# Optimization experiments

Measured on AMD Instinct MI355X. Metric: run time of the kernel, lower is better.

The kernel has to match this reference:

```python
import jax, jax.numpy as jnp
import numpy as np

EPS = 1e-12  # F.normalize eps

def _l2norm(v, axis):
    n = jnp.sqrt(jnp.sum(v * v, axis=axis, keepdims=True))
    return v / jnp.maximum(n, EPS)

def setup_inputs() -> dict:
    key = jax.random.key(0)
    k1, k2, k3, k4 = jax.random.split(key, 4)
    B, C, H, W, K = 8, 1024, 64, 64, 64
    x = jax.random.normal(k1, (B, C, H, W), dtype=jnp.float32)
    centroids = jax.random.normal(k2, (K, C), dtype=jnp.float32)
    # 1x1 conv initialized to identity in the module; use random perturbed weights for a non-trivial test
    fc_weight = jax.random.normal(k3, (C, C), dtype=jnp.float32) * 0.02 + jnp.eye(C, dtype=jnp.float32)
    fc_bias = jax.random.normal(k4, (C,), dtype=jnp.float32) * 0.01
    return {"x": x, "centroids": centroids, "fc_weight": fc_weight, "fc_bias": fc_bias}

def reference(x, centroids, fc_weight, fc_bias):
    B, C, H, W = x.shape
    K = centroids.shape[0]
    # Eq.1: nearest-centroid assignment via cosine similarity
    x_n = _l2norm(x, axis=1)            # [B,C,H,W]
    g_n = _l2norm(centroids, axis=1)    # [K,C]
    sim = jnp.einsum('bchw,nc->bnhw', x_n, g_n)          # [B,K,H,W]
    idx = jnp.argmax(sim, axis=1)                        # [B,H,W]
    assign = jax.nn.one_hot(idx, K, dtype=x.dtype)       # [B,H,W,K]
    # Eq.2: batch-wise local centroids
    sum_x = jnp.einsum('bhwn,bchw->bnc', assign, x)      # [B,K,C]
    count = jnp.sum(assign, axis=(1, 2))[..., None]      # [B,K,1]
    centroids_local = sum_x / jnp.maximum(count, 1.0)    # [B,K,C]
    # Eq.3,4: calibration
    lk_map = jnp.einsum('bhwn,bnc->bchw', assign, centroids_local)  # [B,C,H,W]
    delta = lk_map - x
    w = jnp.exp(-jnp.mean(delta * delta, axis=1, keepdims=True))    # [B,1,H,W]
    x_cal = x + w * delta
    # 1x1 conv + relu
    out = jnp.einsum('oc,bchw->bohw', fc_weight, x_cal) + fc_bias[None, :, None, None]
    return jax.nn.relu(out)
```

## Files before the change

kernel.cpp:

```cpp
#include <hip/hip_runtime.h>
#include <stdint.h>

#define B_   8
#define C_   1024
#define HW_  4096
#define K_   64
#define NPIX (B_*HW_)
#define SLAB ((size_t)B_*K_*C_)
#define NSEG 8

typedef __attribute__((ext_vector_type(8))) short short8;
typedef __attribute__((ext_vector_type(4))) float f32x4;

__device__ __forceinline__ uint16_t f2bf(float f) {
  uint32_t u = __float_as_uint(f);
  u += 0x7fffu + ((u >> 16) & 1u);
  return (uint16_t)(u >> 16);
}

__device__ __forceinline__ void gl2lds16(const uint16_t* g, uint16_t* l) {
  __builtin_amdgcn_global_load_lds(
      (const __attribute__((address_space(1))) unsigned int*)(g),
      (__attribute__((address_space(3))) unsigned int*)(l), 16, 0, 0);
}

__global__ void prep_gT(const float* __restrict__ g, float* __restrict__ gT) {
  int n = blockIdx.x;
  int t = threadIdx.x;
  float vals[4]; float ss = 0.f;
  #pragma unroll
  for (int i = 0; i < 4; i++) { float v = g[n*C_ + t + i*256]; vals[i] = v; ss += v*v; }
  __shared__ float red[256];
  red[t] = ss; __syncthreads();
  for (int s = 128; s > 0; s >>= 1) { if (t < s) red[t] += red[t+s]; __syncthreads(); }
  float scale = 1.f / fmaxf(sqrtf(red[0]), 1e-12f);
  #pragma unroll
  for (int i = 0; i < 4; i++) gT[(t + i*256)*K_ + n] = vals[i]*scale;
}

__global__ void prep_wb(const float* __restrict__ w, uint16_t* __restrict__ wb) {
  int i = blockIdx.x*256 + threadIdx.x;
  float4 v = *(const float4*)&w[i*4];
  uint16_t o[4] = {f2bf(v.x), f2bf(v.y), f2bf(v.z), f2bf(v.w)};
  *(uint64_t*)&wb[i*4] = *(const uint64_t*)o;
}

__launch_bounds__(256)
__global__ void pass_assign(const float* __restrict__ x, const float* __restrict__ gT,
                            int* __restrict__ idx, int* __restrict__ count) {
  int bb = blockIdx.x >> 6;
  int pt = blockIdx.x & 63;
  int t = threadIdx.x;
  int lane = t & 63;
  int ng = __builtin_amdgcn_readfirstlane(t >> 6);
  const float* xp = x + (size_t)bb*C_*HW_ + pt*64 + lane;
  const float* gp = gT + ng*16;
  float acc[16];
  #pragma unroll
  for (int n = 0; n < 16; n++) acc[n] = 0.f;

  float xa[8], xb2[8];
  #pragma unroll
  for (int u = 0; u < 8; u++) xa[u] = xp[(size_t)u*HW_];
  for (int cb = 0; cb < C_; cb += 16) {
    #pragma unroll
    for (int u = 0; u < 8; u++) xb2[u] = xp[(size_t)(cb + 8 + u)*HW_];
    #pragma unroll
    for (int u = 0; u < 8; u++) {
      const float* gr = gp + (cb + u)*K_;
      #pragma unroll
      for (int n = 0; n < 16; n++) acc[n] = fmaf(xa[u], gr[n], acc[n]);
    }
    if (cb + 16 < C_) {
      #pragma unroll
      for (int u = 0; u < 8; u++) xa[u] = xp[(size_t)(cb + 16 + u)*HW_];
    }
    #pragma unroll
    for (int u = 0; u < 8; u++) {
      const float* gr = gp + (cb + 8 + u)*K_;
      #pragma unroll
      for (int n = 0; n < 16; n++) acc[n] = fmaf(xb2[u], gr[n], acc[n]);
    }
  }

  float best = acc[0]; int bi = 0;
  #pragma unroll
  for (int n = 1; n < 16; n++) { if (acc[n] > best) { best = acc[n]; bi = n; } }
  __shared__ float bv[4][64];
  __shared__ int   bn[4][64];
  __shared__ int   hist[64];
  if (t < 64) hist[t] = 0;
  bv[ng][lane] = best; bn[ng][lane] = ng*16 + bi;
  __syncthreads();
  if (t < 64) {
    float mv = bv[0][t]; int mn = bn[0][t];
    #pragma unroll
    for (int wv2 = 1; wv2 < 4; wv2++) { if (bv[wv2][t] > mv) { mv = bv[wv2][t]; mn = bn[wv2][t]; } }
    idx[bb*HW_ + pt*64 + t] = mn;
    atomicAdd(&hist[mn], 1);
  }
  __syncthreads();
  if (t < 64 && hist[t] > 0) atomicAdd(&count[bb*K_ + t], hist[t]);
}

__launch_bounds__(256)
__global__ void pass_bins(const float* __restrict__ x, const int* __restrict__ idx,
                          float* __restrict__ sumxp) {
  int bid = blockIdx.x;
  int ps = bid & 7;
  int ct = (bid >> 3) & 15;
  int bb = bid >> 7;
  int t = threadIdx.x;
  int lane = t & 63;
  int w = t >> 6;
  int col = lane & 15;
  int kg  = lane >> 4;
  int crow = ct*64 + w*16 + col;
  const float* xp = x + (size_t)bb*C_*HW_ + (size_t)crow*HW_ + ps*512 + kg*8;
  const int*   ip = idx + bb*HW_ + ps*512 + kg*8;

  const f32x4 fzero = {0.f, 0.f, 0.f, 0.f};
  f32x4 acc[4];
  #pragma unroll
  for (int f = 0; f < 4; f++) acc[f] = fzero;

  for (int ks = 0; ks < 16; ks++) {
    float a0[8];
    *(float4*)&a0[0] = *(const float4*)&xp[ks*32];
    *(float4*)&a0[4] = *(const float4*)&xp[ks*32 + 4];
    short8 af;
    #pragma unroll
    for (int j = 0; j < 8; j++) af[j] = (short)f2bf(a0[j]);
    int iv8[8];
    *(int4*)&iv8[0] = *(const int4*)&ip[ks*32];
    *(int4*)&iv8[4] = *(const int4*)&ip[ks*32 + 4];
    #pragma unroll
    for (int f = 0; f < 4; f++) {
      int n = f*16 + col;
      short8 bfrag;
      #pragma unroll
      for (int j = 0; j < 8; j++) bfrag[j] = (short)((iv8[j] == n) ? 0x3F80 : 0);
      acc[f] = __builtin_amdgcn_mfma_f32_16x16x32_bf16(af, bfrag, acc[f], 0, 0, 0);
    }
  }
  #pragma unroll
  for (int f = 0; f < 4; f++) {
    int n = f*16 + col;
    size_t base = (size_t)ps*SLAB + ((size_t)bb*K_ + n)*C_ + ct*64 + w*16 + kg*4;
    *(f32x4*)&sumxp[base] = acc[f];
  }
}

__launch_bounds__(256)
__global__ void pass_cfinal(const float* __restrict__ sumxp, const int* __restrict__ count,
                            float* __restrict__ cl, float* __restrict__ clT,
                            float* __restrict__ cn2) {
  int bb = blockIdx.x >> 6, n = blockIdx.x & 63, t = threadIdx.x;
  float inv = 1.f / fmaxf((float)count[bb*K_ + n], 1.f);
  float ss = 0.f;
  #pragma unroll
  for (int i = 0; i < 4; i++) {
    int c = t + i*256;
    size_t o = ((size_t)bb*K_ + n)*C_ + c;
    float v = 0.f;
    #pragma unroll
    for (int s = 0; s < NSEG; s++) v += sumxp[o + (size_t)s*SLAB];
    v *= inv;
    cl [((size_t)bb*K_ + n)*C_ + c] = v;
    clT[((size_t)bb*C_ + c)*K_ + n] = v;
    ss += v*v;
  }
  __shared__ float red[256];
  red[t] = ss; __syncthreads();
  for (int s = 128; s > 0; s >>= 1) { if (t < s) red[t] += red[t+s]; __syncthreads(); }
  if (t == 0) cn2[bb*K_ + n] = red[0];
}

__launch_bounds__(256)
__global__ void pass_xcal(const float* __restrict__ x, const int* __restrict__ idx,
                          const float* __restrict__ cl, const float* __restrict__ clT,
                          const float* __restrict__ cn2, uint16_t* __restrict__ xcal) {
  int bb = blockIdx.x >> 6, pt = blockIdx.x & 63, t = threadIdx.x;
  int lane = t & 63, cs = t >> 6;
  __shared__ float xT[64][129];
  __shared__ int   widx[64];
  __shared__ float pdot[4][64], pxsq[4][64], wv[64];
  if (t < 64) widx[t] = idx[bb*HW_ + pt*64 + t];
  __syncthreads();
  const float* xb = x + (size_t)bb*C_*HW_ + pt*64;
  int myi = widx[lane];
  const float* clb = clT + (size_t)bb*C_*K_ + myi;
  float dp = 0.f, xq = 0.f;
  #pragma unroll 4
  for (int ci = 0; ci < 256; ci++) {
    int c = cs*256 + ci;
    float xv = xb[(size_t)c*HW_ + lane];
    dp = fmaf(xv, clb[(size_t)c*K_], dp);
    xq = fmaf(xv, xv, xq);
  }
  pdot[cs][lane] = dp; pxsq[cs][lane] = xq;
  __syncthreads();
  if (t < 64) {
    float d = pdot[0][t]+pdot[1][t]+pdot[2][t]+pdot[3][t];
    float q = pxsq[0][t]+pxsq[1][t]+pxsq[2][t]+pxsq[3][t];
    float msd = (q - 2.f*d + cn2[bb*K_ + widx[t]]) * (1.f/1024.f);
    wv[t] = expf(-msd);
  }
  __syncthreads();
  for (int cc = 0; cc < 8; cc++) {
    #pragma unroll
    for (int i = 0; i < 32; i++) {
      int co = cs*32 + i;
      xT[lane][co] = xb[(size_t)(cc*128 + co)*HW_ + lane];
    }
    __syncthreads();
    #pragma unroll 2
    for (int pp = 0; pp < 16; pp++) {
      int p = pp*4 + cs;
      float wval = wv[p]; int iv = widx[p];
      const float* clr = cl + ((size_t)bb*K_ + iv)*C_ + cc*128;
      size_t obase = ((size_t)(bb*HW_ + pt*64 + p))*C_ + cc*128;
      #pragma unroll
      for (int ci = 0; ci < 2; ci++) {
        int co = ci*64 + lane;
        float xvv = xT[p][co];
        float v = fmaf(wval, clr[co] - xvv, xvv);
        xcal[obase + co] = f2bf(v);
      }
    }
    __syncthreads();
  }
}

#define BK 64
__launch_bounds__(256)
__global__ void gemm_out(const uint16_t* __restrict__ wb, const uint16_t* __restrict__ xcal,
                         const float* __restrict__ bias, float* __restrict__ out) {
  __shared__ alignas(16) uint16_t smem[2*2*128*BK];
  float* ep = (float*)smem;
  int t = threadIdx.x;
  int lane = t & 63;
  int w = t >> 6, wm = w & 1, wn = w >> 1;
  int g  = blockIdx.x & 7;
  int li = blockIdx.x >> 3;
  int ot = li & 7;
  int qt = g*32 + (li >> 3);

  const uint16_t* wsrc = wb   + (size_t)ot*128*C_;
  const uint16_t* xsrc = xcal + (size_t)qt*128*C_;

  const f32x4 fzero = {0.f, 0.f, 0.f, 0.f};
  f32x4 acc[4][4];
  #pragma unroll
  for (int i = 0; i < 4; i++)
    #pragma unroll
    for (int j = 0; j < 4; j++) acc[i][j] = fzero;

  auto STAGE = [&](int buf, int kb) {
    uint16_t* lw = smem + (size_t)buf*2*128*BK;
    uint16_t* lx = lw + 128*BK;
    #pragma unroll
    for (int it = 0; it < 4; it++) {
      int s = t + it*256;
      int r = s >> 3, q = s & 7;
      int qm = q ^ (r & 7);
      uint16_t* ldw = lw + (size_t)(it*256 + w*64)*8;
      uint16_t* ldx = lx + (size_t)(it*256 + w*64)*8;
      gl2lds16(wsrc + (size_t)r*C_ + kb*BK + qm*8, ldw);
      gl2lds16(xsrc + (size_t)r*C_ + kb*BK + qm*8, ldx);
    }
  };

  STAGE(0, 0);
  __syncthreads();
  for (int kb = 0; kb < C_/BK; kb++) {
    int cur = kb & 1;
    if (kb + 1 < C_/BK) STAGE(cur ^ 1, kb + 1);
    const uint16_t* lw = smem + (size_t)cur*2*128*BK;
    const uint16_t* lx = lw + 128*BK;
    #pragma unroll
    for (int kk = 0; kk < 2; kk++) {
      short8 af[4], bf[4];
      #pragma unroll
      for (int i = 0; i < 4; i++) {
        int row = wm*64 + i*16 + (lane & 15);
        int q = kk*4 + (lane >> 4);
        af[i] = *(const short8*)&lw[row*BK + (q ^ (row & 7))*8];
      }
      #pragma unroll
      for (int j = 0; j < 4; j++) {
        int row = wn*64 + j*16 + (lane & 15);
        int q = kk*4 + (lane >> 4);
        bf[j] = *(const short8*)&lx[row*BK + (q ^ (row & 7))*8];
      }
      #pragma unroll
      for (int i = 0; i < 4; i++)
        #pragma unroll
        for (int j = 0; j < 4; j++)
          acc[i][j] = __builtin_amdgcn_mfma_f32_16x16x32_bf16(af[i], bf[j], acc[i][j], 0, 0, 0);
    }
    __syncthreads();
  }
  int col = lane & 15, quad = lane >> 4;
  int bq = (qt*128) >> 12;
  int p0 = (qt*128) & 4095;
  #pragma unroll
  for (int ph = 0; ph < 2; ph++) {
    if (wm == ph) {
      #pragma unroll
      for (int i = 0; i < 4; i++)
        #pragma unroll
        for (int j = 0; j < 4; j++) {
          int p = wn*64 + j*16 + col;
          #pragma unroll
          for (int r = 0; r < 4; r++) {
            int o2 = i*16 + quad*4 + r;
            ep[o2*128 + (((p >> 2) ^ (o2 & 7)) << 2) + (p & 3)] = acc[i][j][r];
          }
        }
    }
    __syncthreads();
    #pragma unroll
    for (int i2 = 0; i2 < 8; i2++) {
      int s = t + i2*256;
      int ol = s >> 5, pf = s & 31;
      float4 v = *(const float4*)&ep[ol*128 + ((pf ^ (ol & 7)) << 2)];
      int o = ot*128 + ph*64 + ol;
      float bi = bias[o];
      v.x = fmaxf(v.x + bi, 0.f); v.y = fmaxf(v.y + bi, 0.f);
      v.z = fmaxf(v.z + bi, 0.f); v.w = fmaxf(v.w + bi, 0.f);
      *(float4*)&out[(size_t)bq*C_*HW_ + (size_t)o*HW_ + p0 + pf*4] = v;
    }
    __syncthreads();
  }
}

extern "C" void kernel_launch(void* const* d_in, const int* in_sizes, int n_in,
                              void* d_out, int out_size, void* d_ws, size_t ws_size,
                              hipStream_t stream) {
  (void)in_sizes; (void)n_in; (void)out_size; (void)ws_size;
  const float* x    = (const float*)d_in[0];
  const float* cent = (const float*)d_in[1];
  const float* fw   = (const float*)d_in[2];
  const float* fb   = (const float*)d_in[3];
  float* out = (float*)d_out;
  char* ws = (char*)d_ws;
  size_t off = 0;
  float*    gT    = (float*)(ws + off);    off += (size_t)C_*K_*4;
  int*      idx   = (int*)(ws + off);      off += (size_t)NPIX*4;
  int*      count = (int*)(ws + off);      off += (size_t)B_*K_*4;
  float*    sumx  = (float*)(ws + off);    off += (size_t)B_*K_*C_*4;
  float*    cl    = (float*)(ws + off);    off += (size_t)B_*K_*C_*4;
  float*    clT   = (float*)(ws + off);    off += (size_t)B_*C_*K_*4;
  float*    cn2   = (float*)(ws + off);    off += (size_t)B_*K_*4 + 8;
  uint16_t* wb    = (uint16_t*)(ws + off); off += (size_t)C_*C_*2;
  uint16_t* xcal  = (uint16_t*)(ws + off); off += (size_t)NPIX*C_*2;
  (void)sumx;
  float* sumxp = (float*)xcal;

  hipMemsetAsync(count, 0, (size_t)B_*K_*4, stream);
  prep_gT   <<<64,   256, 0, stream>>>(cent, gT);
  prep_wb   <<<1024, 256, 0, stream>>>(fw, wb);
  pass_assign<<<512, 256, 0, stream>>>(x, gT, idx, count);
  pass_bins <<<1024, 256, 0, stream>>>(x, idx, sumxp);
  pass_cfinal<<<512, 256, 0, stream>>>(sumxp, count, cl, clT, cn2);
  pass_xcal <<<512,  256, 0, stream>>>(x, idx, cl, clT, cn2, xcal);
  gemm_out  <<<2048, 256, 0, stream>>>(wb, xcal, fb, out);
}
```

Baseline: 534.2 us.

## Stage x tiles through double-buffered LDS in assignment pass to share loads

The assignment kernel previously had each of the four waves independently load the same 64-pixel x columns from global memory (scalar loads, 4x redundant). Now the block cooperatively loads 32-channel x tiles with float4 loads into a double-buffered shared-memory array, and each wave reads its x values from LDS while the next tile is prefetched. This cuts global/L2 traffic for x by sharing across waves, at the cost of a barrier per 32-channel chunk and extra LDS reads.

Result: faster. 492.8 us (-7.7%).

```diff
diff --git a/kernel.cpp b/kernel.cpp
--- a/kernel.cpp
+++ b/kernel.cpp
@@ -52,35 +52,47 @@
   int pt = blockIdx.x & 63;
   int t = threadIdx.x;
   int lane = t & 63;
-  int ng = __builtin_amdgcn_readfirstlane(t >> 6);
-  const float* xp = x + (size_t)bb*C_*HW_ + pt*64 + lane;
+  int w = t >> 6;
+  int ng = __builtin_amdgcn_readfirstlane(w);
+  __shared__ alignas(16) float xs[2][32][64];
+  const float* xb = x + (size_t)bb*C_*HW_ + pt*64;
   const float* gp = gT + ng*16;
+
+  int r0 = t >> 4;
+  int q0 = t & 15;
+  const float* p0 = xb + (size_t)r0*HW_ + q0*4;
+  const float* p1 = p0 + (size_t)16*HW_;
+
   float acc[16];
   #pragma unroll
   for (int n = 0; n < 16; n++) acc[n] = 0.f;
 
-  float xa[8], xb2[8];
-  #pragma unroll
-  for (int u = 0; u < 8; u++) xa[u] = xp[(size_t)u*HW_];
-  for (int cb = 0; cb < C_; cb += 16) {
-    #pragma unroll
-    for (int u = 0; u < 8; u++) xb2[u] = xp[(size_t)(cb + 8 + u)*HW_];
-    #pragma unroll
-    for (int u = 0; u < 8; u++) {
-      const float* gr = gp + (cb + u)*K_;
-      #pragma unroll
-      for (int n = 0; n < 16; n++) acc[n] = fmaf(xa[u], gr[n], acc[n]);
-    }
-    if (cb + 16 < C_) {
-      #pragma unroll
-      for (int u = 0; u < 8; u++) xa[u] = xp[(size_t)(cb + 16 + u)*HW_];
-    }
-    #pragma unroll
-    for (int u = 0; u < 8; u++) {
-      const float* gr = gp + (cb + 8 + u)*K_;
-      #pragma unroll
-      for (int n = 0; n < 16; n++) acc[n] = fmaf(xb2[u], gr[n], acc[n]);
-    }
+  {
+    float4 v0 = *(const float4*)p0;
+    float4 v1 = *(const float4*)p1;
+    *(float4*)&xs[0][r0][q0*4]    = v0;
+    *(float4*)&xs[0][r0+16][q0*4] = v1;
+  }
+  __syncthreads();
+  for (int cc = 0; cc < 32; cc++) {
+    int cur = cc & 1;
+    float4 n0, n1;
+    if (cc + 1 < 32) {
+      n0 = *(const float4*)(p0 + (size_t)(cc + 1)*32*HW_);
+      n1 = *(const float4*)(p1 + (size_t)(cc + 1)*32*HW_);
+    }
+    #pragma unroll 16
+    for (int ci = 0; ci < 32; ci++) {
+      float xv = xs[cur][ci][lane];
+      const float* gr = gp + (cc*32 + ci)*K_;
+      #pragma unroll
+      for (int n2 = 0; n2 < 16; n2++) acc[n2] = fmaf(xv, gr[n2], acc[n2]);
+    }
+    if (cc + 1 < 32) {
+      *(float4*)&xs[cur^1][r0][q0*4]    = n0;
+      *(float4*)&xs[cur^1][r0+16][q0*4] = n1;
+    }
+    __syncthreads();
   }
 
   float best = acc[0]; int bi = 0;
@@ -90,7 +102,7 @@
   __shared__ int   bn[4][64];
   __shared__ int   hist[64];
   if (t < 64) hist[t] = 0;
-  bv[ng][lane] = best; bn[ng][lane] = ng*16 + bi;
+  bv[w][lane] = best; bn[w][lane] = ng*16 + bi;
   __syncthreads();
   if (t < 64) {
     float mv = bv[0][t]; int mn = bn[0][t];
```
